# Optimization experiments

Hardware: AMD Instinct MI355X
Metric: run time of the kernel (lower is better)

The kernel has to match this reference:

```python
import jax, jax.numpy as jnp
import numpy as np

ALPHA, GAMMA = 0.25, 2.0
MD_THRES = 0.5
BF, AF, VAR = 1.0, 0.5, 1.0  # mining_param chosen to exercise the DAS (dynamic anchor selection) path
BETA = 1.0 / 9.0
EPS = 1e-8


def rbox_corners(boxes):
    # boxes [N,5] = (cx, cy, w, h, angle_deg) -> corners [N,4,2]
    cx, cy, w, h, a = (boxes[:, i] for i in range(5))
    t = a * (jnp.pi / 180.0)
    c, s = jnp.cos(t), jnp.sin(t)
    lx = jnp.array([-0.5, 0.5, 0.5, -0.5], boxes.dtype)
    ly = jnp.array([-0.5, -0.5, 0.5, 0.5], boxes.dtype)
    dx = w[:, None] * lx[None, :]
    dy = h[:, None] * ly[None, :]
    x = cx[:, None] + dx * c[:, None] - dy * s[:, None]
    y = cy[:, None] + dx * s[:, None] + dy * c[:, None]
    return jnp.stack([x, y], axis=-1)


def _pts_in_poly(pts, poly):
    # pts [P,2], poly [4,2] convex quad -> [P] bool
    e = jnp.roll(poly, -1, axis=0) - poly
    rel = pts[:, None, :] - poly[None, :, :]
    cr = e[None, :, 0] * rel[:, :, 1] - e[None, :, 1] * rel[:, :, 0]
    return jnp.all(cr >= -1e-6, axis=1) | jnp.all(cr <= 1e-6, axis=1)


def _pair_inter_area(ca, cb):
    # exact convex quad-quad intersection area; ca, cb: [4,2]
    p, q = ca, cb
    r = jnp.roll(ca, -1, axis=0) - ca
    s = jnp.roll(cb, -1, axis=0) - cb
    rxs = r[:, None, 0] * s[None, :, 1] - r[:, None, 1] * s[None, :, 0]  # [4,4]
    qp = q[None, :, :] - p[:, None, :]
    qpxs = qp[..., 0] * s[None, :, 1] - qp[..., 1] * s[None, :, 0]
    qpxr = qp[..., 0] * r[:, None, 1] - qp[..., 1] * r[:, None, 0]
    denom = jnp.where(jnp.abs(rxs) > 1e-10, rxs, 1.0)
    t = qpxs / denom
    u = qpxr / denom
    valid = (jnp.abs(rxs) > 1e-10) & (t >= 0) & (t <= 1) & (u >= 0) & (u <= 1)
    ipts = p[:, None, :] + t[..., None] * r[:, None, :]  # [4,4,2]
    cand = jnp.concatenate([ca, cb, ipts.reshape(16, 2)], axis=0)  # [24,2]
    mask = jnp.concatenate([_pts_in_poly(ca, cb), _pts_in_poly(cb, ca), valid.reshape(16)])
    n = mask.sum()
    center = (cand * mask[:, None]).sum(0) / jnp.maximum(n, 1)
    d = cand - center
    ang = jnp.where(mask, jnp.arctan2(d[:, 1], d[:, 0]), 1e9)
    order = jnp.argsort(ang)  # valid points first, CCW order
    sp = cand[order]
    sm = mask[order]
    sp = jnp.where(sm[:, None], sp, sp[0])  # pad with first vertex (zero shoelace contribution)
    nx = jnp.roll(sp, -1, axis=0)
    area = 0.5 * jnp.abs(jnp.sum(sp[:, 0] * nx[:, 1] - nx[:, 0] * sp[:, 1]))
    return jnp.where(n >= 3, area, 0.0)


def rbox_iou(boxes_a, boxes_b, indicator, thresh=0.1):
    # exact rotated IoU, computed only where axis-aligned indicator >= thresh (else 0)
    ca = rbox_corners(boxes_a)
    cb = rbox_corners(boxes_b)
    inter = jax.vmap(lambda a: jax.vmap(lambda b: _pair_inter_area(a, b))(cb))(ca)  # [N,M]
    area_a = (boxes_a[:, 2] * boxes_a[:, 3])[:, None]
    area_b = (boxes_b[:, 2] * boxes_b[:, 3])[None, :]
    iou = inter / (area_a + area_b - inter + EPS)
    return jnp.where(indicator >= thresh, iou, 0.0)


def min_area_square(rb):
    s = jnp.maximum(rb[:, 2], rb[:, 3]) * 0.5
    return jnp.stack([rb[:, 0] - s, rb[:, 1] - s, rb[:, 0] + s, rb[:, 1] + s], axis=1)


def bbox_overlaps(a, b):
    # axis-aligned IoU, a [N,4], b [M,4] (xyxy)
    lt = jnp.maximum(a[:, None, :2], b[None, :, :2])
    rb = jnp.minimum(a[:, None, 2:], b[None, :, 2:])
    wh = jnp.clip(rb - lt, 0.0)
    inter = wh[..., 0] * wh[..., 1]
    aa = (a[:, 2] - a[:, 0]) * (a[:, 3] - a[:, 1])
    ab = (b[:, 2] - b[:, 0]) * (b[:, 3] - b[:, 1])
    return inter / (aa[:, None] + ab[None, :] - inter + EPS)


def box_encode(ex, gt):
    gw = jnp.maximum(gt[:, 2], 1.0)
    gh = jnp.maximum(gt[:, 3], 1.0)
    dx = (gt[:, 0] - ex[:, 0]) / ex[:, 2]
    dy = (gt[:, 1] - ex[:, 1]) / ex[:, 3]
    dw = jnp.log(gw / ex[:, 2])
    dh = jnp.log(gh / ex[:, 3])
    dt = jnp.tan(gt[:, 4] * jnp.pi / 180.0) - jnp.tan(ex[:, 4] * jnp.pi / 180.0)
    return jnp.stack([dx, dy, dw, dh, dt], axis=1)


def _image_loss(cls, reg, anc, ranc, ann):
    A, C = cls.shape
    M = ann.shape[0]
    gt = ann[:, :5]
    labels = ann[:, 5].astype(jnp.int32)
    cls = jnp.clip(cls, 1e-4, 1.0 - 1e-4)
    ov_bf = rbox_iou(anc, gt, bbox_overlaps(min_area_square(anc), min_area_square(gt)))
    ov_af = rbox_iou(ranc, gt, bbox_overlaps(min_area_square(ranc), min_area_square(gt)))
    md = jnp.abs(BF * ov_bf + AF * ov_af - jnp.abs(ov_af - ov_bf) ** VAR)
    md = jax.lax.stop_gradient(md)  # original computes overlaps via numpy (no grad)
    iou_max = md.max(1)
    iou_argmax = md.argmax(1)
    pos = iou_max >= MD_THRES
    max_gt = md.max(0)
    argmax_gt = md.argmax(0)
    force = jnp.zeros((A,), jnp.int32).at[argmax_gt].add((max_gt < MD_THRES).astype(jnp.int32)) > 0
    pos = pos | force
    num_pos = pos.sum()
    # DAS matching weights (rows only meaningful at positive anchors; computed full + masked)
    md_p = jnp.where(pos[:, None], md, -jnp.inf)
    max_pos = md_p.max(0)   # [M]
    arg_pos = md_p.argmax(0)
    pos_mask = (md >= MD_THRES) & pos[:, None]
    pos_mask = pos_mask.at[arg_pos, jnp.arange(M)].set(True)
    comp = jnp.where(pos_mask, 1.0 - max_pos[None, :], md)
    mw_max = (comp + md).max(1)  # matching_weight.max(1)[0]
    # classification targets: -1 ignore / 0 neg / 1 pos-class
    assigned = gt[iou_argmax]
    alab = labels[iou_argmax]
    onehot = alab[:, None] == jnp.arange(C)[None, :]
    tgt = jnp.broadcast_to(jnp.where(iou_max < MD_THRES - 0.1, 0.0, -1.0)[:, None], (A, C))
    tgt = jnp.where(pos[:, None], 0.0, tgt)
    tgt = jnp.where(pos[:, None] & onehot, 1.0, tgt)
    af = jnp.where(tgt == 1.0, ALPHA, 1.0 - ALPHA)
    fw = af * jnp.where(tgt == 1.0, 1.0 - cls, cls) ** GAMMA
    bce = -(tgt * jnp.log(cls + 1e-6) + (1.0 - tgt) * jnp.log(1.0 - cls + 1e-6))
    sw = jnp.where(tgt == 0.0, 1.0, 0.0)
    sw = jnp.where(pos[:, None] & onehot, mw_max[:, None] + 1.0, sw)
    cls_loss = jnp.where(tgt != -1.0, fw * bce * sw, 0.0)
    cls_l = cls_loss.sum() / jnp.maximum(num_pos.astype(cls.dtype), 1.0)
    reg_t = box_encode(anc, assigned)
    diff = jnp.abs(reg - reg_t)
    sl1 = jnp.where(diff < BETA, 0.5 * diff ** 2 / BETA, diff - 0.5 * BETA) * mw_max[:, None]
    sl1 = jnp.where(pos[:, None], sl1, 0.0)
    reg_l = jnp.where(num_pos > 0, sl1.sum() / jnp.maximum(num_pos * 5, 1).astype(cls.dtype), 0.0)
    return cls_l, reg_l


def _forward(classifications, regressions, anchors, refined_achors, annotations):
    B = classifications.shape[0]
    cl, rl = [], []
    for j in range(B):  # small fixed batch loop, as in the original
        c, r = _image_loss(classifications[j], regressions[j], anchors[j], refined_achors[j], annotations[j])
        cl.append(c)
        rl.append(r)
    loss_cls = jnp.stack(cl).mean(keepdims=True)
    loss_reg = jnp.stack(rl).mean(keepdims=True)
    return loss_cls, loss_reg


def _rand_boxes(key, shape):
    k1, k2, k3, k4, k5 = jax.random.split(key, 5)
    cx = jax.random.uniform(k1, shape, minval=32.0, maxval=992.0)
    cy = jax.random.uniform(k2, shape, minval=32.0, maxval=992.0)
    w = jax.random.uniform(k3, shape, minval=16.0, maxval=160.0)
    h = jax.random.uniform(k4, shape, minval=16.0, maxval=160.0)
    a = jax.random.uniform(k5, shape, minval=-30.0, maxval=30.0)
    return jnp.stack([cx, cy, w, h, a], axis=-1)


def setup_inputs() -> dict:
    key = jax.random.key(0)
    ks = jax.random.split(key, 6)
    B, A, M, C = 2, 16384, 32, 15
    classifications = jax.random.uniform(ks[0], (B, A, C), minval=0.02, maxval=0.98)
    regressions = 0.1 * jax.random.normal(ks[1], (B, A, 5))
    anchors = _rand_boxes(ks[2], (B, A))
    noise = 0.05 * jax.random.normal(ks[3], (B, A, 5))
    refined_achors = anchors + noise * jnp.array([8.0, 8.0, 4.0, 4.0, 5.0])
    gt = _rand_boxes(ks[4], (B, M))
    labels = jax.random.randint(ks[5], (B, M, 1), 0, C).astype(jnp.float32)
    annotations = jnp.concatenate([gt, labels], axis=-1)  # all labels valid (!= -1)
    return {"classifications": classifications, "regressions": regressions, "anchors": anchors,
            "refined_achors": refined_achors, "annotations": annotations}


def reference(classifications, regressions, anchors, refined_achors, annotations):
    return _forward(classifications, regressions, anchors, refined_achors, annotations)
```

## Files before the change

kernel.cpp:

```cpp
#include <hip/hip_runtime.h>
#include <math.h>

typedef unsigned long long u64;
typedef unsigned int u32;

static constexpr int A = 16384;
static constexpr int M = 32;
static constexpr int C = 15;
static constexpr int B = 2;
static constexpr int NBLK = A / 32;
static constexpr int NGATE = B * A * M / 256;
static constexpr int NLOSS = (A / 256) * B;
static constexpr int KPAD = 16;

static constexpr double PI_D = 3.14159265358979323846;

static constexpr size_t OFF_MD     = 0;
static constexpr size_t OFF_LIST   = OFF_MD + (size_t)B*A*M*4;
static constexpr size_t OFF_SEGC   = OFF_LIST + (size_t)NGATE*256*4;
static constexpr size_t OFF_KEYALL = OFF_SEGC + (size_t)NGATE*4;
static constexpr size_t OFF_KEYPOS = OFF_KEYALL + (size_t)B*M*KPAD*8;
static constexpr size_t OFF_IOUMAX = OFF_KEYPOS + (size_t)B*M*KPAD*8;
static constexpr size_t OFF_IOUARG = OFF_IOUMAX + (size_t)B*A*4;
static constexpr size_t OFF_POS    = OFF_IOUARG + (size_t)B*A*4;
static constexpr size_t OFF_NUMPOS = OFF_POS + (size_t)B*A*4;
static constexpr size_t OFF_NPFIX  = OFF_NUMPOS + (size_t)B*4;
static constexpr size_t OFF_SUMS   = (OFF_NPFIX + (size_t)B*4 + 7) & ~(size_t)7;
static constexpr size_t OFF_DONES  = OFF_SUMS + 4*8;

__device__ inline double aa_square_iou(double cx1, double cy1, double s1,
                                       double cx2, double cy2, double s2) {
    double lx = fmax(cx1 - s1, cx2 - s2), ly = fmax(cy1 - s1, cy2 - s2);
    double rx = fmin(cx1 + s1, cx2 + s2), ry = fmin(cy1 + s1, cy2 + s2);
    double w = fmax(rx - lx, 0.0), h = fmax(ry - ly, 0.0);
    double inter = w * h;
    double aa = (2.0 * s1) * (2.0 * s1);
    double ab = (2.0 * s2) * (2.0 * s2);
    return inter / (aa + ab - inter + 1e-8);
}

__device__ inline void rbox_corners1(double cx, double cy, double w, double h,
                                     double adeg, double* X, double* Y) {
    double t = adeg * (PI_D / 180.0);
    double c = cos(t), s = sin(t);
    const double lx[4] = {-0.5, 0.5, 0.5, -0.5};
    const double ly[4] = {-0.5, -0.5, 0.5, 0.5};
#pragma unroll
    for (int i = 0; i < 4; ++i) {
        double dx = w * lx[i], dy = h * ly[i];
        X[i] = cx + dx * c - dy * s;
        Y[i] = cy + dx * s + dy * c;
    }
}

__device__ inline double edges_in_quad_cross_sum(const double* PX, const double* PY,
                                                 const double* QX, const double* QY) {
    double s = 0.0;
#pragma unroll
    for (int k = 0; k < 4; ++k) {
        double x0 = PX[k], y0 = PY[k];
        double x1 = PX[(k + 1) & 3], y1 = PY[(k + 1) & 3];
        double ex = x1 - x0, ey = y1 - y0;
        double t0 = 0.0, t1 = 1.0;
        bool empty = false;
#pragma unroll
        for (int e = 0; e < 4; ++e) {
            double qx0 = QX[e], qy0 = QY[e];
            double qex = QX[(e + 1) & 3] - qx0;
            double qey = QY[(e + 1) & 3] - qy0;
            double d0 = qex * (y0 - qy0) - qey * (x0 - qx0);
            double d1 = qex * (y1 - qy0) - qey * (x1 - qx0);
            if (d0 < 0.0 && d1 < 0.0) empty = true;
            else if (d0 < 0.0) t0 = fmax(t0, d0 / (d0 - d1));
            else if (d1 < 0.0) t1 = fmin(t1, d0 / (d0 - d1));
        }
        if (!empty && t1 > t0) {
            double ax = x0 + t0 * ex, ay = y0 + t0 * ey;
            double bx = x0 + t1 * ex, by = y0 + t1 * ey;
            s += ax * by - ay * bx;
        }
    }
    return s;
}

__device__ inline double quad_inter_area(const double* AX, const double* AY,
                                         const double* BX, const double* BY) {
    double s = edges_in_quad_cross_sum(AX, AY, BX, BY) +
               edges_in_quad_cross_sum(BX, BY, AX, AY);
    return 0.5 * fabs(s);
}

__device__ inline u64 pack_key(float v, u32 inv_idx) {
    return ((u64)__float_as_uint(v) << 32) | (u64)inv_idx;
}

__global__ void k_gate(const float* __restrict__ anc, const float* __restrict__ ranc,
                       const float* __restrict__ ann, float* __restrict__ md,
                       u32* __restrict__ list, u32* __restrict__ segcnt,
                       u64* __restrict__ keyAll, u64* __restrict__ keyPos,
                       int* __restrict__ num_pos, double* __restrict__ sums,
                       int* __restrict__ dones) {
    __shared__ u32 l_cnt;
    __shared__ u32 l_idx[256];
    int tid = threadIdx.x;
    if (tid == 0) l_cnt = 0;
    __syncthreads();

    int t = blockIdx.x * 256 + tid;
    if (t < B * M * KPAD) { keyAll[t] = 0ull; keyPos[t] = 0ull; }
    if (t < 4) sums[t] = 0.0;
    if (t < 2) num_pos[t] = 0;
    if (t < 1) dones[0] = 0;
    int m = t & (M - 1);
    int a = (t >> 5) & (A - 1);
    int b = t >> 19;

    const float* pa = anc + ((size_t)(b * A + a)) * 5;
    const float* pr = ranc + ((size_t)(b * A + a)) * 5;
    const float* pg = ann + ((size_t)(b * M + m)) * 6;

    double cxg = pg[0], cyg = pg[1];
    double sg = 0.5 * fmax((double)pg[2], (double)pg[3]);
    double i_bf = aa_square_iou(pa[0], pa[1], 0.5 * fmax((double)pa[2], (double)pa[3]),
                                cxg, cyg, sg);
    double i_af = aa_square_iou(pr[0], pr[1], 0.5 * fmax((double)pr[2], (double)pr[3]),
                                cxg, cyg, sg);
    bool g = (i_bf >= 0.1) || (i_af >= 0.1);
    md[t] = 0.0f;

    if (g) {
        u32 s = atomicAdd(&l_cnt, 1u);
        l_idx[s] = (u32)t;
    }
    __syncthreads();
    u32 n = l_cnt;
    if ((u32)tid < n) list[blockIdx.x * 256 + tid] = l_idx[tid];
    if (tid == 0) segcnt[blockIdx.x] = n;
}

__global__ void k_geom(const float* __restrict__ anc, const float* __restrict__ ranc,
                       const float* __restrict__ ann, const u32* __restrict__ list,
                       const u32* __restrict__ segcnt, float* __restrict__ md) {
    int gtid = blockIdx.x * 256 + threadIdx.x;
    int wave = gtid >> 6;
    int lane = gtid & 63;
    u32 n = segcnt[wave];
    for (u32 i = lane; i < n; i += 64) {
        u32 t = list[wave * 256 + i];
        int m = t & (M - 1);
        int a = ((int)t >> 5) & (A - 1);
        int b = (int)t >> 19;
        const float* pa = anc + ((size_t)(b * A + a)) * 5;
        const float* pr = ranc + ((size_t)(b * A + a)) * 5;
        const float* pg = ann + ((size_t)(b * M + m)) * 6;

        double cxg = pg[0], cyg = pg[1], wg = pg[2], hg = pg[3], ag = pg[4];
        double sg = 0.5 * fmax(wg, hg);
        double cxa = pa[0], cya = pa[1], wa = pa[2], ha = pa[3], aa = pa[4];
        double cxr = pr[0], cyr = pr[1], wr = pr[2], hr = pr[3], ar = pr[4];

        double i_bf = aa_square_iou(cxa, cya, 0.5 * fmax(wa, ha), cxg, cyg, sg);
        double i_af = aa_square_iou(cxr, cyr, 0.5 * fmax(wr, hr), cxg, cyg, sg);

        double GX[4], GY[4];
        rbox_corners1(cxg, cyg, wg, hg, ag, GX, GY);
        double areaG = wg * hg;
        double ov_bf = 0.0, ov_af = 0.0;
        if (i_bf >= 0.1) {
            double X[4], Y[4];
            rbox_corners1(cxa, cya, wa, ha, aa, X, Y);
            double inter = quad_inter_area(X, Y, GX, GY);
            ov_bf = inter / (wa * ha + areaG - inter + 1e-8);
        }
        if (i_af >= 0.1) {
            double X[4], Y[4];
            rbox_corners1(cxr, cyr, wr, hr, ar, X, Y);
            double inter = quad_inter_area(X, Y, GX, GY);
            ov_af = inter / (wr * hr + areaG - inter + 1e-8);
        }
        md[t] = (float)fabs(ov_bf + 0.5 * ov_af - fabs(ov_af - ov_bf));
    }
}

__global__ void k_assign(const float* __restrict__ md,
                         float* __restrict__ iou_max, int* __restrict__ iou_arg,
                         int* __restrict__ pos, u64* __restrict__ keyAll,
                         u64* __restrict__ keyPos, int* __restrict__ num_pos) {
    int blk = blockIdx.x, b = blockIdx.y, tid = threadIdx.x;
    int a0 = blk * 32;
    const float4* src = (const float4*)(md + (size_t)(b * A + a0) * M);
    float4 v4 = src[tid];
    int rr = tid >> 3, c0 = (tid & 7) * 4;
    float vv[4] = {v4.x, v4.y, v4.z, v4.w};

    u64 rowk = 0;
#pragma unroll
    for (int j = 0; j < 4; ++j) {
        u64 k = pack_key(vv[j], 0xFFFFFFFFu - (u32)(c0 + j));
        if (k > rowk) rowk = k;
    }
#pragma unroll
    for (int off = 1; off < 8; off <<= 1) {
        u64 o = __shfl_xor(rowk, off, 8);
        if (o > rowk) rowk = o;
    }
    float rmax = __uint_as_float((u32)(rowk >> 32));
    int p = (rmax >= 0.5f) ? 1 : 0;

    __shared__ u64 lAll[32][33];
    __shared__ u64 lPos[32][33];
    __shared__ int lcnt[32];
    u32 inva = 0xFFFFFFFFu - (u32)(a0 + rr);
#pragma unroll
    for (int j = 0; j < 4; ++j) {
        u64 ck = pack_key(vv[j], inva);
        lAll[rr][c0 + j] = ck;
        lPos[rr][c0 + j] = p ? ck : 0ull;
    }
    if ((tid & 7) == 0) {
        int idx = b * A + a0 + rr;
        iou_max[idx] = rmax;
        iou_arg[idx] = (int)(0xFFFFFFFFu - (u32)(rowk & 0xFFFFFFFFull));
        pos[idx] = p;
        lcnt[rr] = p;
    }
    __syncthreads();
    if (tid < 32) {
        u64 ka = 0, kp = 0;
#pragma unroll
        for (int r = 0; r < 32; ++r) {
            u64 x = lAll[r][tid]; if (x > ka) ka = x;
            u64 y = lPos[r][tid]; if (y > kp) kp = y;
        }
        atomicMax(&keyAll[(b * M + tid) * KPAD], ka);
        if (kp) atomicMax(&keyPos[(b * M + tid) * KPAD], kp);
        if (tid == 0) {
            int c = 0;
#pragma unroll
            for (int r = 0; r < 32; ++r) c += lcnt[r];
            if (c) atomicAdd(&num_pos[b], c);
        }
    }
}

__global__ void k_loss(const float* __restrict__ cls_in, const float* __restrict__ reg_in,
                       const float* __restrict__ anc, const float* __restrict__ ann,
                       const float* __restrict__ md,
                       const float* __restrict__ iou_max, const int* __restrict__ iou_arg,
                       const int* __restrict__ pos,
                       const u64* __restrict__ keyAll, const u64* __restrict__ keyPos,
                       const int* __restrict__ num_pos, int* __restrict__ npfix,
                       double* __restrict__ sums, int* __restrict__ dones,
                       float* __restrict__ out) {
    int b = blockIdx.y;
    int tid = threadIdx.x;
    int a = blockIdx.x * 256 + tid;

    __shared__ int s_fl[M];
    __shared__ float s_maxpos[M];
    __shared__ int s_argpos[M];
    if (tid < M) {
        u64 kall = keyAll[(b * M + tid) * KPAD];
        float mx = __uint_as_float((u32)(kall >> 32));
        s_fl[tid] = (mx < 0.5f) ? (int)(0xFFFFFFFFu - (u32)(kall & 0xFFFFFFFFull)) : -1;
    }
    __syncthreads();
    if (tid < M) {
        u64 kp = keyPos[(b * M + tid) * KPAD];
        for (int f = 0; f < M; ++f) {
            int fa = s_fl[f];
            if (fa >= 0) {
                float v = md[((size_t)(b * A + fa)) * M + tid];
                u64 k = pack_key(v, 0xFFFFFFFFu - (u32)fa);
                if (k > kp) kp = k;
            }
        }
        if (kp == 0ull) { s_maxpos[tid] = 0.0f; s_argpos[tid] = -1; }
        else {
            s_maxpos[tid] = __uint_as_float((u32)(kp >> 32));
            s_argpos[tid] = (int)(0xFFFFFFFFu - (u32)(kp & 0xFFFFFFFFull));
        }
    }
    __syncthreads();

    if (blockIdx.x == 0 && tid == 0) {
        int np = num_pos[b];
        for (int f = 0; f < M; ++f) {
            int fa = s_fl[f];
            if (fa < 0 || pos[b * A + fa] != 0) continue;
            bool dup = false;
            for (int f2 = 0; f2 < f; ++f2) if (s_fl[f2] == fa) { dup = true; break; }
            if (!dup) ++np;
        }
        atomicExch(&npfix[b], np);
    }

    double csum = 0.0, rsum = 0.0;
    {
        int t = b * A + a;
        float imax = iou_max[t];
        int iarg = iou_arg[t];
        int p = pos[t];
        for (int f = 0; f < M; ++f) if (a == s_fl[f]) p = 1;

        float mwf;
        if (p) {
            const float* row = md + (size_t)t * M;
            mwf = -INFINITY;
#pragma unroll
            for (int m = 0; m < M; ++m) {
                float v = row[m];
                bool pm = (v >= 0.5f) || (a == s_argpos[m]);
                float val = pm ? (1.0f - s_maxpos[m] + v) : (v + v);
                mwf = fmaxf(mwf, val);
            }
        } else {
            mwf = imax + imax;
        }
        double mw = (double)mwf;

        const float* g = ann + ((size_t)(b * M + iarg)) * 6;
        int lab = (int)g[5];
        const float* cp = cls_in + (size_t)t * C;
#pragma unroll
        for (int c = 0; c < C; ++c) {
            double x = (double)cp[c];
            x = fmin(fmax(x, 1e-4), 1.0 - 1e-4);
            double tgt;
            if (p) tgt = (c == lab) ? 1.0 : 0.0;
            else   tgt = (imax < 0.4f) ? 0.0 : -1.0;
            if (tgt >= 0.0) {
                bool one = (tgt == 1.0);
                double af = one ? 0.25 : 0.75;
                double q = one ? (1.0 - x) : x;
                double fw = af * q * q;
                double bce = one ? -log(x + 1e-6) : -log(1.0 - x + 1e-6);
                double sw = one ? (mw + 1.0) : 1.0;
                csum += fw * bce * sw;
            }
        }
        if (p) {
            const float* pa = anc + (size_t)t * 5;
            double gw = fmax((double)g[2], 1.0);
            double gh = fmax((double)g[3], 1.0);
            double rt0 = ((double)g[0] - (double)pa[0]) / (double)pa[2];
            double rt1 = ((double)g[1] - (double)pa[1]) / (double)pa[3];
            double rt2 = log(gw / (double)pa[2]);
            double rt3 = log(gh / (double)pa[3]);
            double rt4 = tan((double)g[4] * (PI_D / 180.0)) - tan((double)pa[4] * (PI_D / 180.0));
            double rt[5] = {rt0, rt1, rt2, rt3, rt4};
            const float* rg = reg_in + (size_t)t * 5;
#pragma unroll
            for (int k = 0; k < 5; ++k) {
                double d = fabs((double)rg[k] - rt[k]);
                double s = (d < (1.0 / 9.0)) ? (0.5 * d * d * 9.0) : (d - 0.5 / 9.0);
                rsum += s * mw;
            }
        }
    }
    __shared__ double scs[256];
    __shared__ double srs[256];
    scs[tid] = csum;
    srs[tid] = rsum;
    __syncthreads();
    for (int s = 128; s > 0; s >>= 1) {
        if (tid < s) { scs[tid] += scs[tid + s]; srs[tid] += srs[tid + s]; }
        __syncthreads();
    }
    if (tid == 0) {
        atomicAdd(&sums[b], scs[0]);
        atomicAdd(&sums[2 + b], srs[0]);
    }

    __syncthreads();
    __shared__ int s_last;
    if (tid == 0) s_last = (atomicAdd(&dones[0], 1) == NLOSS - 1) ? 1 : 0;
    __syncthreads();
    if (s_last && tid == 0) {
        double lc = 0.0, lr = 0.0;
        for (int bb = 0; bb < B; ++bb) {
            int np = __hip_atomic_load(&npfix[bb], __ATOMIC_RELAXED, __HIP_MEMORY_SCOPE_AGENT);
            double sc = __hip_atomic_load(&sums[bb], __ATOMIC_RELAXED, __HIP_MEMORY_SCOPE_AGENT);
            double sr = __hip_atomic_load(&sums[2 + bb], __ATOMIC_RELAXED, __HIP_MEMORY_SCOPE_AGENT);
            lc += sc / fmax((double)np, 1.0);
            int denom = np * 5;
            if (denom < 1) denom = 1;
            lr += (np > 0) ? (sr / (double)denom) : 0.0;
        }
        out[0] = (float)(lc / (double)B);
        out[1] = (float)(lr / (double)B);
    }
}

extern "C" void kernel_launch(void* const* d_in, const int* in_sizes, int n_in,
                              void* d_out, int out_size, void* d_ws, size_t ws_size,
                              hipStream_t stream) {
    const float* cls  = (const float*)d_in[0];
    const float* reg  = (const float*)d_in[1];
    const float* anc  = (const float*)d_in[2];
    const float* ranc = (const float*)d_in[3];
    const float* ann  = (const float*)d_in[4];
    float* out = (float*)d_out;

    char* ws = (char*)d_ws;
    float* md      = (float*)(ws + OFF_MD);
    u32*   list    = (u32*)(ws + OFF_LIST);
    u32*   segcnt  = (u32*)(ws + OFF_SEGC);
    u64*   keyAll  = (u64*)(ws + OFF_KEYALL);
    u64*   keyPos  = (u64*)(ws + OFF_KEYPOS);
    float* iou_max = (float*)(ws + OFF_IOUMAX);
    int*   iou_arg = (int*)(ws + OFF_IOUARG);
    int*   pos     = (int*)(ws + OFF_POS);
    int*   num_pos = (int*)(ws + OFF_NUMPOS);
    int*   npfix   = (int*)(ws + OFF_NPFIX);
    double* sums   = (double*)(ws + OFF_SUMS);
    int*   dones   = (int*)(ws + OFF_DONES);

    (void)in_sizes; (void)n_in; (void)out_size; (void)ws_size;

    k_gate<<<NGATE, 256, 0, stream>>>(anc, ranc, ann, md, list, segcnt,
                                      keyAll, keyPos, num_pos, sums, dones);
    k_geom<<<NGATE / 4, 256, 0, stream>>>(anc, ranc, ann, list, segcnt, md);
    k_assign<<<dim3(NBLK, B), 256, 0, stream>>>(md, iou_max, iou_arg, pos,
                                                keyAll, keyPos, num_pos);
    k_loss<<<dim3(A / 256, B), 256, 0, stream>>>(cls, reg, anc, ann, md, iou_max,
                                                 iou_arg, pos, keyAll, keyPos,
                                                 num_pos, npfix, sums, dones, out);
}
```

Baseline: 125.9 us.

## Fuse per-anchor assignment into geometry kernel and count positives in loss kernel

```diff
diff --git a/kernel.cpp b/kernel.cpp
--- a/kernel.cpp
+++ b/kernel.cpp
@@ -8,9 +8,8 @@
 static constexpr int M = 32;
 static constexpr int C = 15;
 static constexpr int B = 2;
-static constexpr int NBLK = A / 32;
 static constexpr int NGATE = B * A * M / 256;
-static constexpr int NLOSS = (A / 256) * B;
+static constexpr int NLOSS = (A / 128) * B;
 static constexpr int KPAD = 16;
 
 static constexpr double PI_D = 3.14159265358979323846;
@@ -22,10 +21,8 @@
 static constexpr size_t OFF_KEYPOS = OFF_KEYALL + (size_t)B*M*KPAD*8;
 static constexpr size_t OFF_IOUMAX = OFF_KEYPOS + (size_t)B*M*KPAD*8;
 static constexpr size_t OFF_IOUARG = OFF_IOUMAX + (size_t)B*A*4;
-static constexpr size_t OFF_POS    = OFF_IOUARG + (size_t)B*A*4;
-static constexpr size_t OFF_NUMPOS = OFF_POS + (size_t)B*A*4;
-static constexpr size_t OFF_NPFIX  = OFF_NUMPOS + (size_t)B*4;
-static constexpr size_t OFF_SUMS   = (OFF_NPFIX + (size_t)B*4 + 7) & ~(size_t)7;
+static constexpr size_t OFF_NPC    = OFF_IOUARG + (size_t)B*A*4;
+static constexpr size_t OFF_SUMS   = (OFF_NPC + (size_t)B*4 + 7) & ~(size_t)7;
 static constexpr size_t OFF_DONES  = OFF_SUMS + 4*8;
 
 __device__ inline double aa_square_iou(double cx1, double cy1, double s1,
@@ -98,7 +95,7 @@
                        const float* __restrict__ ann, float* __restrict__ md,
                        u32* __restrict__ list, u32* __restrict__ segcnt,
                        u64* __restrict__ keyAll, u64* __restrict__ keyPos,
-                       int* __restrict__ num_pos, double* __restrict__ sums,
+                       int* __restrict__ npc, double* __restrict__ sums,
                        int* __restrict__ dones) {
     __shared__ u32 l_cnt;
     __shared__ u32 l_idx[256];
@@ -107,9 +104,12 @@
     __syncthreads();
 
     int t = blockIdx.x * 256 + tid;
-    if (t < B * M * KPAD) { keyAll[t] = 0ull; keyPos[t] = 0ull; }
+    if (t < B * M) {
+        keyAll[(size_t)t * KPAD] = pack_key(0.0f, 0xFFFFFFFFu);
+        keyPos[(size_t)t * KPAD] = 0ull;
+    }
     if (t < 4) sums[t] = 0.0;
-    if (t < 2) num_pos[t] = 0;
+    if (t < 2) npc[t] = 0;
     if (t < 1) dones[0] = 0;
     int m = t & (M - 1);
     int a = (t >> 5) & (A - 1);
@@ -140,14 +140,21 @@
 
 __global__ void k_geom(const float* __restrict__ anc, const float* __restrict__ ranc,
                        const float* __restrict__ ann, const u32* __restrict__ list,
-                       const u32* __restrict__ segcnt, float* __restrict__ md) {
-    int gtid = blockIdx.x * 256 + threadIdx.x;
-    int wave = gtid >> 6;
-    int lane = gtid & 63;
-    u32 n = segcnt[wave];
+                       const u32* __restrict__ segcnt, float* __restrict__ md,
+                       u64* __restrict__ keyAll, u64* __restrict__ keyPos,
+                       float* __restrict__ iou_max, int* __restrict__ iou_arg) {
+    __shared__ float rowbuf[4][8][32];
+    int tid = threadIdx.x;
+    int wv = tid >> 6, lane = tid & 63;
+    int seg = blockIdx.x * 4 + wv;
+
+    for (int j = lane; j < 256; j += 64) ((float*)rowbuf[wv])[j] = 0.0f;
+    __syncthreads();
+
+    u32 n = segcnt[seg];
     for (u32 i = lane; i < n; i += 64) {
-        u32 t = list[wave * 256 + i];
-        int m = t & (M - 1);
+        u32 t = list[seg * 256 + i];
+        int m = (int)t & (M - 1);
         int a = ((int)t >> 5) & (A - 1);
         int b = (int)t >> 19;
         const float* pa = anc + ((size_t)(b * A + a)) * 5;
@@ -178,67 +185,34 @@
             double inter = quad_inter_area(X, Y, GX, GY);
             ov_af = inter / (wr * hr + areaG - inter + 1e-8);
         }
-        md[t] = (float)fabs(ov_bf + 0.5 * ov_af - fabs(ov_af - ov_bf));
-    }
-}
-
-__global__ void k_assign(const float* __restrict__ md,
-                         float* __restrict__ iou_max, int* __restrict__ iou_arg,
-                         int* __restrict__ pos, u64* __restrict__ keyAll,
-                         u64* __restrict__ keyPos, int* __restrict__ num_pos) {
-    int blk = blockIdx.x, b = blockIdx.y, tid = threadIdx.x;
-    int a0 = blk * 32;
-    const float4* src = (const float4*)(md + (size_t)(b * A + a0) * M);
-    float4 v4 = src[tid];
-    int rr = tid >> 3, c0 = (tid & 7) * 4;
-    float vv[4] = {v4.x, v4.y, v4.z, v4.w};
-
-    u64 rowk = 0;
-#pragma unroll
-    for (int j = 0; j < 4; ++j) {
-        u64 k = pack_key(vv[j], 0xFFFFFFFFu - (u32)(c0 + j));
-        if (k > rowk) rowk = k;
-    }
-#pragma unroll
-    for (int off = 1; off < 8; off <<= 1) {
-        u64 o = __shfl_xor(rowk, off, 8);
-        if (o > rowk) rowk = o;
-    }
-    float rmax = __uint_as_float((u32)(rowk >> 32));
-    int p = (rmax >= 0.5f) ? 1 : 0;
-
-    __shared__ u64 lAll[32][33];
-    __shared__ u64 lPos[32][33];
-    __shared__ int lcnt[32];
-    u32 inva = 0xFFFFFFFFu - (u32)(a0 + rr);
-#pragma unroll
-    for (int j = 0; j < 4; ++j) {
-        u64 ck = pack_key(vv[j], inva);
-        lAll[rr][c0 + j] = ck;
-        lPos[rr][c0 + j] = p ? ck : 0ull;
-    }
-    if ((tid & 7) == 0) {
-        int idx = b * A + a0 + rr;
-        iou_max[idx] = rmax;
-        iou_arg[idx] = (int)(0xFFFFFFFFu - (u32)(rowk & 0xFFFFFFFFull));
-        pos[idx] = p;
-        lcnt[rr] = p;
-    }
-    __syncthreads();
-    if (tid < 32) {
-        u64 ka = 0, kp = 0;
-#pragma unroll
-        for (int r = 0; r < 32; ++r) {
-            u64 x = lAll[r][tid]; if (x > ka) ka = x;
-            u64 y = lPos[r][tid]; if (y > kp) kp = y;
-        }
-        atomicMax(&keyAll[(b * M + tid) * KPAD], ka);
-        if (kp) atomicMax(&keyPos[(b * M + tid) * KPAD], kp);
-        if (tid == 0) {
-            int c = 0;
-#pragma unroll
-            for (int r = 0; r < 32; ++r) c += lcnt[r];
-            if (c) atomicAdd(&num_pos[b], c);
+        float mdv = (float)fabs(ov_bf + 0.5 * ov_af - fabs(ov_af - ov_bf));
+        md[t] = mdv;
+        rowbuf[wv][((int)t >> 5) & 7][m] = mdv;
+        atomicMax(&keyAll[(size_t)(b * M + m) * KPAD],
+                  pack_key(mdv, 0xFFFFFFFFu - (u32)a));
+    }
+    __syncthreads();
+
+    if (lane < 8) {
+        int ra = seg * 8 + lane;
+        int b = ra >> 14;
+        int a = ra & (A - 1);
+        u64 rowk = 0ull;
+#pragma unroll
+        for (int m = 0; m < M; ++m) {
+            u64 k = pack_key(rowbuf[wv][lane][m], 0xFFFFFFFFu - (u32)m);
+            if (k > rowk) rowk = k;
+        }
+        float rmax = __uint_as_float((u32)(rowk >> 32));
+        iou_max[ra] = rmax;
+        iou_arg[ra] = (int)(0xFFFFFFFFu - (u32)(rowk & 0xFFFFFFFFull));
+        if (rmax >= 0.5f) {
+            u32 inva = 0xFFFFFFFFu - (u32)a;
+#pragma unroll
+            for (int m = 0; m < M; ++m) {
+                atomicMax(&keyPos[(size_t)(b * M + m) * KPAD],
+                          pack_key(rowbuf[wv][lane][m], inva));
+            }
         }
     }
 }
@@ -247,26 +221,25 @@
                        const float* __restrict__ anc, const float* __restrict__ ann,
                        const float* __restrict__ md,
                        const float* __restrict__ iou_max, const int* __restrict__ iou_arg,
-                       const int* __restrict__ pos,
                        const u64* __restrict__ keyAll, const u64* __restrict__ keyPos,
-                       const int* __restrict__ num_pos, int* __restrict__ npfix,
-                       double* __restrict__ sums, int* __restrict__ dones,
-                       float* __restrict__ out) {
+                       int* __restrict__ npc, double* __restrict__ sums,
+                       int* __restrict__ dones, float* __restrict__ out) {
     int b = blockIdx.y;
     int tid = threadIdx.x;
-    int a = blockIdx.x * 256 + tid;
+    int a = blockIdx.x * 128 + tid;
 
     __shared__ int s_fl[M];
     __shared__ float s_maxpos[M];
     __shared__ int s_argpos[M];
     if (tid < M) {
-        u64 kall = keyAll[(b * M + tid) * KPAD];
+        u64 kall = keyAll[(size_t)(b * M + tid) * KPAD];
         float mx = __uint_as_float((u32)(kall >> 32));
         s_fl[tid] = (mx < 0.5f) ? (int)(0xFFFFFFFFu - (u32)(kall & 0xFFFFFFFFull)) : -1;
     }
     __syncthreads();
     if (tid < M) {
-        u64 kp = keyPos[(b * M + tid) * KPAD];
+        u64 kp = keyPos[(size_t)(b * M + tid) * KPAD];
+#pragma unroll
         for (int f = 0; f < M; ++f) {
             int fa = s_fl[f];
             if (fa >= 0) {
@@ -283,24 +256,14 @@
     }
     __syncthreads();
 
-    if (blockIdx.x == 0 && tid == 0) {
-        int np = num_pos[b];
-        for (int f = 0; f < M; ++f) {
-            int fa = s_fl[f];
-            if (fa < 0 || pos[b * A + fa] != 0) continue;
-            bool dup = false;
-            for (int f2 = 0; f2 < f; ++f2) if (s_fl[f2] == fa) { dup = true; break; }
-            if (!dup) ++np;
-        }
-        atomicExch(&npfix[b], np);
-    }
-
     double csum = 0.0, rsum = 0.0;
+    int p;
     {
         int t = b * A + a;
         float imax = iou_max[t];
         int iarg = iou_arg[t];
-        int p = pos[t];
+        p = (imax >= 0.5f) ? 1 : 0;
+#pragma unroll
         for (int f = 0; f < M; ++f) if (a == s_fl[f]) p = 1;
 
         float mwf;
@@ -358,18 +321,25 @@
             }
         }
     }
-    __shared__ double scs[256];
-    __shared__ double srs[256];
+    __shared__ double scs[128];
+    __shared__ double srs[128];
+    __shared__ int sci[128];
     scs[tid] = csum;
     srs[tid] = rsum;
-    __syncthreads();
-    for (int s = 128; s > 0; s >>= 1) {
-        if (tid < s) { scs[tid] += scs[tid + s]; srs[tid] += srs[tid + s]; }
+    sci[tid] = p;
+    __syncthreads();
+    for (int s = 64; s > 0; s >>= 1) {
+        if (tid < s) {
+            scs[tid] += scs[tid + s];
+            srs[tid] += srs[tid + s];
+            sci[tid] += sci[tid + s];
+        }
         __syncthreads();
     }
     if (tid == 0) {
         atomicAdd(&sums[b], scs[0]);
         atomicAdd(&sums[2 + b], srs[0]);
+        if (sci[0]) atomicAdd(&npc[b], sci[0]);
     }
 
     __syncthreads();
@@ -379,7 +349,7 @@
     if (s_last && tid == 0) {
         double lc = 0.0, lr = 0.0;
         for (int bb = 0; bb < B; ++bb) {
-            int np = __hip_atomic_load(&npfix[bb], __ATOMIC_RELAXED, __HIP_MEMORY_SCOPE_AGENT);
+            int np = __hip_atomic_load(&npc[bb], __ATOMIC_RELAXED, __HIP_MEMORY_SCOPE_AGENT);
             double sc = __hip_atomic_load(&sums[bb], __ATOMIC_RELAXED, __HIP_MEMORY_SCOPE_AGENT);
             double sr = __hip_atomic_load(&sums[2 + bb], __ATOMIC_RELAXED, __HIP_MEMORY_SCOPE_AGENT);
             lc += sc / fmax((double)np, 1.0);
@@ -410,20 +380,17 @@
     u64*   keyPos  = (u64*)(ws + OFF_KEYPOS);
     float* iou_max = (float*)(ws + OFF_IOUMAX);
     int*   iou_arg = (int*)(ws + OFF_IOUARG);
-    int*   pos     = (int*)(ws + OFF_POS);
-    int*   num_pos = (int*)(ws + OFF_NUMPOS);
-    int*   npfix   = (int*)(ws + OFF_NPFIX);
+    int*   npc     = (int*)(ws + OFF_NPC);
     double* sums   = (double*)(ws + OFF_SUMS);
     int*   dones   = (int*)(ws + OFF_DONES);
 
     (void)in_sizes; (void)n_in; (void)out_size; (void)ws_size;
 
     k_gate<<<NGATE, 256, 0, stream>>>(anc, ranc, ann, md, list, segcnt,
-                                      keyAll, keyPos, num_pos, sums, dones);
-    k_geom<<<NGATE / 4, 256, 0, stream>>>(anc, ranc, ann, list, segcnt, md);
-    k_assign<<<dim3(NBLK, B), 256, 0, stream>>>(md, iou_max, iou_arg, pos,
-                                                keyAll, keyPos, num_pos);
-    k_loss<<<dim3(A / 256, B), 256, 0, stream>>>(cls, reg, anc, ann, md, iou_max,
-                                                 iou_arg, pos, keyAll, keyPos,
-                                                 num_pos, npfix, sums, dones, out);
-}
+                                      keyAll, keyPos, npc, sums, dones);
+    k_geom<<<NGATE / 4, 256, 0, stream>>>(anc, ranc, ann, list, segcnt, md,
+                                          keyAll, keyPos, iou_max, iou_arg);
+    k_loss<<<dim3(A / 128, B), 128, 0, stream>>>(cls, reg, anc, ann, md, iou_max,
+                                                 iou_arg, keyAll, keyPos,
+                                                 npc, sums, dones, out);
+}
```

Result: slower. 131.8 us (+4.7%).
